# Performance work log

Measured on AMD Instinct MI355X. Metric: run time of the kernel, lower is better.

The kernel has to match this reference:

```python
import jax, jax.numpy as jnp
import numpy as np

N_WIN = 8
NUM_HEADS = 8
TOPK = 4
D_MODEL = 128
SCALE = D_MODEL ** (-0.5)


def setup_inputs() -> dict:
    key = jax.random.key(0)
    k1, k2 = jax.random.split(key)
    cv_feature = jax.random.normal(k1, (1, 128, 128, 128), dtype=jnp.float32)
    mv_feature = jax.random.normal(k2, (1, 2, 128, 128, 128), dtype=jnp.float32)
    return {"cv_feature": cv_feature, "mv_feature": mv_feature}


def reference(cv_feature, mv_feature):
    # cv_feature: [N, H, W, C] query view; mv_feature: [N, V, H, W, C] multi-view KV
    N, H, W, C = cv_feature.shape
    V = mv_feature.shape[1]
    j = i = N_WIN
    h, w = H // j, W // i
    p2, w2 = j * i, h * w
    ch = C // NUM_HEADS  # per-head dim

    # window partition: n (j h) (i w) c -> n (j i) h w c
    cv_patch = cv_feature.reshape(N, j, h, i, w, C).transpose(0, 1, 3, 2, 4, 5).reshape(N, p2, h, w, C)
    mv_patch = mv_feature.reshape(N, V, j, h, i, w, C).transpose(0, 1, 2, 4, 3, 5, 6).reshape(N, V, p2, h, w, C)

    q_pix = cv_patch.reshape(N, p2, w2, C)          # [N, p2, w2, C]
    kv_pix = mv_patch.reshape(N, V, p2, w2, C)      # [N, V, p2, w2, C]

    # window-level descriptors (means) -> routing logits
    q_win = cv_patch.mean(axis=(2, 3))              # [N, p2, C]
    k_win = mv_patch.mean(axis=(3, 4))              # [N, V, p2, C]

    # TopK routing (detached in original; forward math identical)
    k_flat = k_win.reshape(N, V * p2, C)
    attn_logit = jnp.einsum('npc,nqc->npq', q_win * SCALE, k_flat)  # [N, p2, V*p2]
    topk_logit, r_idx = jax.lax.top_k(attn_logit, TOPK)
    r_weight = jax.nn.softmax(topk_logit, axis=-1)  # computed by module, unused downstream

    # KV gather of selected windows: [N, p2, topk, w2, C]
    kv_flat = kv_pix.reshape(N, V * p2, w2, C)
    kv_sel = kv_flat[jnp.arange(N)[:, None, None], r_idx]

    # per-window multi-head attention over topk*w2 gathered tokens
    q = q_pix.reshape(N, p2, w2, NUM_HEADS, ch)
    kv = kv_sel.reshape(N, p2, TOPK * w2, NUM_HEADS, ch)
    attn = jnp.einsum('npwmc,npxmc->npmwx', q * SCALE, kv)  # [N, p2, m, w2, topk*w2]
    attn = jax.nn.softmax(attn, axis=-1)
    out = jnp.einsum('npmwx,npxmc->npwmc', attn, kv)        # [N, p2, w2, m, ch]

    # merge windows back: n (j i) (h w) c -> n (j h) (i w) c
    out = out.reshape(N, j, i, h, w, C).transpose(0, 1, 3, 2, 4, 5).reshape(N, H, W, C)
    return out
```

## Files before the change

### kernel.cpp

```cpp
#include <hip/hip_runtime.h>

#define HH_ 128
#define WW_ 128
#define CC_ 128
#define P2 64
#define W2 256
#define NH 8
#define CH 16
#define NV 2
#define TOPK 4
#define SCALE 0.08838834764831845f
#define SCALE_L2E 0.1275216f
#define CLAMP_L2 28.8539f

typedef unsigned short u16;
typedef unsigned int   u32;
typedef short s8v __attribute__((ext_vector_type(8)));
typedef float f4  __attribute__((ext_vector_type(4)));

#if __has_builtin(__builtin_amdgcn_exp2f)
#define EXP2(x) __builtin_amdgcn_exp2f(x)
#else
#define EXP2(x) exp2f(x)
#endif

union FRAG { uint4 q; u32 u[4]; s8v v; };

__device__ float g_means[(P2 + NV * P2) * CC_];
__device__ int2  g_part[64];
__device__ int   g_mode;
__device__ int   g_amb;

__device__ inline u16 f2b(float v) {
    union { float f; u32 u; } x; x.f = v;
    u32 r = x.u + 0x7FFFu + ((x.u >> 16) & 1u);
    return (u16)(r >> 16);
}
__device__ inline float b2f(u16 h) {
    union { u32 u; float f; } x; x.u = (u32)h << 16; return x.f;
}
__device__ inline float h2f(u16 h) {
    u32 s = (h >> 15) & 1u, e = (h >> 10) & 31u, m = h & 1023u;
    float v;
    if (e == 0)       v = m * 5.9604644775e-8f;
    else if (e == 31) v = 65504.f;
    else { union { u32 u; float f; } x; x.u = ((e + 112u) << 23) | (m << 13); v = x.f; }
    return s ? -v : v;
}
__device__ inline u16 f2h(float v) {
    union { float f; u32 u; } x; x.f = v;
    u32 s = (x.u >> 16) & 0x8000u;
    int  e = (int)((x.u >> 23) & 0xFF) - 112;
    u32  m = x.u & 0x7FFFFF;
    if (e >= 31) return (u16)(s | 0x7BFF);
    if (e <= 0) {
        if (e < -10) return (u16)s;
        m |= 0x800000u;
        int sh = 14 - e;
        u32 r = m >> sh, rem = m & ((1u << sh) - 1u), half = 1u << (sh - 1);
        if (rem > half || (rem == half && (r & 1))) r++;
        return (u16)(s | r);
    }
    u32 r = ((u32)e << 10) | (m >> 13), rem = m & 0x1FFFu;
    if (rem > 0x1000u || (rem == 0x1000u && (r & 1))) r++;
    return (u16)(s | r);
}

__device__ inline u32 pkhi(float a, float b) {
    union { float f; u32 u; } xa, xb; xa.f = a; xb.f = b;
    return (xa.u >> 16) | (xb.u & 0xFFFF0000u);
}
__device__ inline float hipart(float a) {
    union { float f; u32 u; } x; x.f = a; x.u &= 0xFFFF0000u; return x.f;
}

template<int MODE>
__device__ inline float decode1(const void* __restrict__ src, int off) {
    if (MODE == 0) return ((const float*)src)[off];
    u16 h = ((const u16*)src)[off];
    return (MODE == 1) ? b2f(h) : h2f(h);
}

template<int MODE>
__device__ inline float4 loadf4(const void* __restrict__ src, int off) {
    if (MODE == 0) return *(const float4*)((const float*)src + off);
    uint2 v = *(const uint2*)((const u16*)src + off);
    float4 r;
    if (MODE == 1) {
        r.x = b2f((u16)v.x); r.y = b2f((u16)(v.x >> 16));
        r.z = b2f((u16)v.y); r.w = b2f((u16)(v.y >> 16));
    } else {
        r.x = h2f((u16)v.x); r.y = h2f((u16)(v.x >> 16));
        r.z = h2f((u16)v.y); r.w = h2f((u16)(v.y >> 16));
    }
    return r;
}

template<int MODE>
__device__ inline void store4t(void* __restrict__ out, int off, const float* __restrict__ r) {
    if (MODE == 0) {
        *(float4*)((float*)out + off) = make_float4(r[0], r[1], r[2], r[3]);
    } else if (MODE == 1) {
        u32 w0 = (u32)f2b(r[0]) | ((u32)f2b(r[1]) << 16);
        u32 w1 = (u32)f2b(r[2]) | ((u32)f2b(r[3]) << 16);
        *(uint2*)((u16*)out + off) = make_uint2(w0, w1);
    } else {
        u32 w0 = (u32)f2h(r[0]) | ((u32)f2h(r[1]) << 16);
        u32 w1 = (u32)f2h(r[2]) | ((u32)f2h(r[3]) << 16);
        *(uint2*)((u16*)out + off) = make_uint2(w0, w1);
    }
}

__global__ void detect_sample(const void* __restrict__ cv, int n) {
    __shared__ int bc[2];
    int tid = threadIdx.x, k = blockIdx.x;
    if (tid < 2) bc[tid] = 0;
    __syncthreads();
    int lim32 = n / 2;
    int lim16 = n / 2;
    u32 r = ((u32)(tid + k * 257) * 2654435761u);
    int j32 = (int)(r % (u32)lim32);
    float a = fabsf(((const float*)cv)[j32]);
    bool c0 = (a >= 1e-4f && a <= 1e4f);
    int j16 = 2 * (int)((r >> 8) % (u32)lim16);
    float b = fabsf(b2f(((const u16*)cv)[j16]));
    bool c1 = (b >= 1e-4f && b <= 1e4f);
    unsigned long long b0 = __ballot(c0);
    unsigned long long b1 = __ballot(c1);
    if ((tid & 63) == 0) {
        atomicAdd(&bc[0], __popcll(b0));
        atomicAdd(&bc[1], __popcll(b1));
    }
    __syncthreads();
    if (tid == 0) g_part[k] = make_int2(bc[0], bc[1]);
}

__global__ void detect_final() {
    int tid = threadIdx.x;
    int2 v = g_part[tid];
    int c0 = v.x, c1 = v.y;
#pragma unroll
    for (int off = 32; off >= 1; off >>= 1) {
        c0 += __shfl_down(c0, off);
        c1 += __shfl_down(c1, off);
    }
    if (tid == 0) {
        const float T = 256.f * 64.f;
        float f0 = c0 / T, f1 = c1 / T;
        int mode, amb = 0;
        if (f1 >= 0.85f) mode = 1;
        else if (f0 >= 0.80f) mode = 0;
        else mode = 2;
        if ((f1 > 0.60f && f1 < 0.85f) || (mode != 1 && f0 > 0.65f && f0 < 0.80f)) amb = 1;
        g_mode = mode; g_amb = amb;
    }
}

template<int MODE>
__device__ inline void wm_accum(const void* __restrict__ src, int voff, int jj, int ii,
                                int pc, int c0, float* __restrict__ acc) {
#pragma unroll
    for (int k = 0; k < 8; ++k) {
        int px = 8 * pc + k;
        int hh = px >> 4, ww = px & 15;
        int a = voff + ((jj * 16 + hh) * WW_ + ii * 16 + ww) * CC_ + c0;
        if (MODE == 0) {
            const float4* p4 = (const float4*)((const float*)src + a);
            float4 x = p4[0], y = p4[1];
            acc[0] += x.x; acc[1] += x.y; acc[2] += x.z; acc[3] += x.w;
            acc[4] += y.x; acc[5] += y.y; acc[6] += y.z; acc[7] += y.w;
        } else {
            uint4 v = *(const uint4*)((const u16*)src + a);
            u32 wd[4] = { v.x, v.y, v.z, v.w };
#pragma unroll
            for (int j = 0; j < 4; ++j) {
                u16 lo = (u16)(wd[j] & 0xFFFFu), hi = (u16)(wd[j] >> 16);
                acc[2 * j]     += (MODE == 1) ? b2f(lo) : h2f(lo);
                acc[2 * j + 1] += (MODE == 1) ? b2f(hi) : h2f(hi);
            }
        }
    }
}

__global__ __launch_bounds__(512) void win_mean_kernel(const void* __restrict__ cv,
                                                       const void* __restrict__ mv) {
    __shared__ float part[32][128];
    int mode = g_mode;
    int row = blockIdx.x, tid = threadIdx.x;
    int o = tid & 15, pc = tid >> 4;
    const void* src; int voff = 0; int p;
    if (row < P2) { p = row; src = cv; }
    else { int r = row - P2; voff = (r >> 6) * HH_ * WW_ * CC_; p = r & 63; src = mv; }
    int jj = p >> 3, ii = p & 7;
    int c0 = 8 * o;
    float acc[8];
#pragma unroll
    for (int j = 0; j < 8; ++j) acc[j] = 0.f;
    if (mode == 0)      wm_accum<0>(src, voff, jj, ii, pc, c0, acc);
    else if (mode == 1) wm_accum<1>(src, voff, jj, ii, pc, c0, acc);
    else                wm_accum<2>(src, voff, jj, ii, pc, c0, acc);
#pragma unroll
    for (int j = 0; j < 8; ++j) part[pc][c0 + j] = acc[j];
    __syncthreads();
    if (tid < 128) {
        float s = 0.f;
#pragma unroll
        for (int k = 0; k < 32; ++k) s += part[k][tid];
        g_means[row * CC_ + tid] = s * (1.0f / 256.0f);
    }
}

template<int MODE>
__device__ void attn_body(const void* __restrict__ cv, const void* __restrict__ mv,
                          void* __restrict__ out, int p, int m, int tid,
                          u32 (* __restrict__ kfrag)[64][4],
                          u32 (* __restrict__ vfrag)[64][4],
                          const int* __restrict__ rwin) {
    int jj = p >> 3, ii = p & 7;
    int wv = tid >> 6, l = tid & 63;
    int lg = l >> 4, lr = l & 15;

    FRAG qf1[2], qf2[2];
#pragma unroll
    for (int qi = 0; qi < 2; ++qi) {
        int qrow = wv * 32 + qi * 16 + lr;
        int hh = qrow >> 4, ww = qrow & 15;
        int pix = (jj * 16 + hh) * WW_ + (ii * 16 + ww);
        float4 qv = loadf4<MODE>(cv, pix * CC_ + m * CH + 4 * lg);
        float q0 = qv.x * SCALE_L2E, q1 = qv.y * SCALE_L2E;
        float q2 = qv.z * SCALE_L2E, q3 = qv.w * SCALE_L2E;
        u32 h01 = pkhi(q0, q1), h23 = pkhi(q2, q3);
        u32 l01 = pkhi(q0 - hipart(q0), q1 - hipart(q1));
        u32 l23 = pkhi(q2 - hipart(q2), q3 - hipart(q3));
        qf1[qi].u[0] = h01; qf1[qi].u[1] = h23; qf1[qi].u[2] = l01; qf1[qi].u[3] = l23;
        qf2[qi].u[0] = l01; qf2[qi].u[1] = l23; qf2[qi].u[2] = h01; qf2[qi].u[3] = h23;
    }

    int ktl0 = tid >> 6;
    float4 kraw[2];
    float  vraw[2][4];

    auto loadh = [&](int r) {
        int t = rwin[r]; int v = t >> 6, pp = t & 63;
        int jj2 = pp >> 3, ii2 = pp & 7;
        int wrow = (v * HH_ + jj2 * 16) * WW_ + ii2 * 16;
        int kbr = (wrow + lr) * CC_ + m * CH + 4 * lg;
        int vbr = (wrow + 4 * lg) * CC_ + m * CH + lr;
#pragma unroll
        for (int i = 0; i < 2; ++i) {
            int ktl = ktl0 + 8 * i;
            kraw[i] = loadf4<MODE>(mv, kbr + ktl * (WW_ * CC_));
        }
#pragma unroll
        for (int i = 0; i < 2; ++i) {
            int ktl = ktl0 + 8 * i;
            int a = vbr + ktl * (WW_ * CC_);
#pragma unroll
            for (int io = 0; io < 4; ++io)
                vraw[i][io] = decode1<MODE>(mv, a + io * CC_);
        }
    };

    auto writeh = [&]() {
#pragma unroll
        for (int i = 0; i < 2; ++i) {
            int ktl = ktl0 + 8 * i;
            float4 kc = kraw[i];
            FRAG kf;
            kf.u[0] = pkhi(kc.x, kc.y);
            kf.u[1] = pkhi(kc.z, kc.w);
            kf.u[2] = pkhi(kc.x - hipart(kc.x), kc.y - hipart(kc.y));
            kf.u[3] = pkhi(kc.z - hipart(kc.z), kc.w - hipart(kc.w));
            *(uint4*)&kfrag[ktl][l][0] = kf.q;
            float v0 = vraw[i][0], v1 = vraw[i][1], v2 = vraw[i][2], v3 = vraw[i][3];
            FRAG vf;
            vf.u[0] = pkhi(v0, v1);
            vf.u[1] = pkhi(v2, v3);
            vf.u[2] = pkhi(v0 - hipart(v0), v1 - hipart(v1));
            vf.u[3] = pkhi(v2 - hipart(v2), v3 - hipart(v3));
            *(uint4*)&vfrag[ktl][l][0] = vf.q;
        }
    };

    f4 Oacc0 = {0.f, 0.f, 0.f, 0.f};
    f4 Oacc1 = {0.f, 0.f, 0.f, 0.f};
    float lp0 = 0.f, lp1 = 0.f;
    const uint4* kp = (const uint4*)&kfrag[0][0][0] + l;
    const uint4* vp = (const uint4*)&vfrag[0][0][0] + l;

    auto computeh = [&]() {
#pragma unroll 4
        for (int ktl = 0; ktl < 16; ++ktl) {
            FRAG kf, vf;
            kf.q = kp[ktl * 64];
            vf.q = vp[ktl * 64];
            {
                f4 sc = {0.f, 0.f, 0.f, 0.f};
                sc = __builtin_amdgcn_mfma_f32_16x16x32_bf16(kf.v, qf1[0].v, sc, 0, 0, 0);
                sc = __builtin_amdgcn_mfma_f32_16x16x32_bf16(kf.v, qf2[0].v, sc, 0, 0, 0);
                float pe0 = EXP2(fminf(sc[0], CLAMP_L2));
                float pe1 = EXP2(fminf(sc[1], CLAMP_L2));
                float pe2 = EXP2(fminf(sc[2], CLAMP_L2));
                float pe3 = EXP2(fminf(sc[3], CLAMP_L2));
                lp0 += (hipart(pe0) + hipart(pe1)) + (hipart(pe2) + hipart(pe3));
                FRAG pf;
                pf.u[0] = pkhi(pe0, pe1);
                pf.u[1] = pkhi(pe2, pe3);
                pf.u[2] = pf.u[0];
                pf.u[3] = pf.u[1];
                Oacc0 = __builtin_amdgcn_mfma_f32_16x16x32_bf16(vf.v, pf.v, Oacc0, 0, 0, 0);
            }
            {
                f4 sc = {0.f, 0.f, 0.f, 0.f};
                sc = __builtin_amdgcn_mfma_f32_16x16x32_bf16(kf.v, qf1[1].v, sc, 0, 0, 0);
                sc = __builtin_amdgcn_mfma_f32_16x16x32_bf16(kf.v, qf2[1].v, sc, 0, 0, 0);
                float pe0 = EXP2(fminf(sc[0], CLAMP_L2));
                float pe1 = EXP2(fminf(sc[1], CLAMP_L2));
                float pe2 = EXP2(fminf(sc[2], CLAMP_L2));
                float pe3 = EXP2(fminf(sc[3], CLAMP_L2));
                lp1 += (hipart(pe0) + hipart(pe1)) + (hipart(pe2) + hipart(pe3));
                FRAG pf;
                pf.u[0] = pkhi(pe0, pe1);
                pf.u[1] = pkhi(pe2, pe3);
                pf.u[2] = pf.u[0];
                pf.u[3] = pf.u[1];
                Oacc1 = __builtin_amdgcn_mfma_f32_16x16x32_bf16(vf.v, pf.v, Oacc1, 0, 0, 0);
            }
        }
    };

    loadh(0);
    writeh();
    __syncthreads();
#pragma unroll 1
    for (int r = 1; r < 4; ++r) {
        loadh(r);
        computeh();
        __syncthreads();
        writeh();
        __syncthreads();
    }
    computeh();

#pragma unroll
    for (int qi = 0; qi < 2; ++qi) {
        float lt = (qi == 0) ? lp0 : lp1;
        lt += __shfl_xor(lt, 16);
        lt += __shfl_xor(lt, 32);
        float inv = 1.0f / fmaxf(lt, 1e-30f);
        f4 Oa = (qi == 0) ? Oacc0 : Oacc1;
        float res[4];
#pragma unroll
        for (int r = 0; r < 4; ++r)
            res[r] = fminf(fmaxf(Oa[r] * inv, -1000.f), 1000.f);
        int qrow = wv * 32 + qi * 16 + lr;
        int hh = qrow >> 4, ww = qrow & 15;
        int pix = (jj * 16 + hh) * WW_ + (ii * 16 + ww);
        store4t<MODE>(out, pix * CC_ + m * CH + 4 * lg, res);
    }
}

__global__ __launch_bounds__(512, 6) void attn_kernel(const void* __restrict__ cv,
                                                      const void* __restrict__ mv,
                                                      void* __restrict__ out) {
    __shared__ u32 kfrag[16][64][4];
    __shared__ u32 vfrag[16][64][4];
    __shared__ float slog[NV * P2];
    __shared__ int   sridx[TOPK];

    int mode = g_mode;
    int p = blockIdx.x >> 3, m = blockIdx.x & 7;
    int tid = threadIdx.x;

    {
        int t  = tid >> 2;
        int cs = (tid & 3) << 5;
        const float4* qw = (const float4*)(g_means + p * CC_ + cs);
        const float4* kw = (const float4*)(g_means + (P2 + t) * CC_ + cs);
        float a = 0.f;
#pragma unroll
        for (int i = 0; i < 8; ++i) {
            float4 qv = qw[i], kv4 = kw[i];
            a += qv.x * kv4.x + qv.y * kv4.y + qv.z * kv4.z + qv.w * kv4.w;
        }
        a += __shfl_down(a, 2, 4);
        a += __shfl_down(a, 1, 4);
        if ((tid & 3) == 0) slog[t] = a;
    }
    __syncthreads();
    if (tid == 0) {
#pragma unroll
        for (int k = 0; k < TOPK; ++k) {
            int best = 0; float bv = slog[0];
            for (int q2 = 1; q2 < NV * P2; ++q2)
                if (slog[q2] > bv) { bv = slog[q2]; best = q2; }
            sridx[k] = best;
            slog[best] = -3.0e38f;
        }
    }
    __syncthreads();

    int rwin[TOPK];
#pragma unroll
    for (int k = 0; k < TOPK; ++k) rwin[k] = sridx[k] & 127;

    if (mode == 0)      attn_body<0>(cv, mv, out, p, m, tid, kfrag, vfrag, rwin);
    else if (mode == 1) attn_body<1>(cv, mv, out, p, m, tid, kfrag, vfrag, rwin);
    else                attn_body<2>(cv, mv, out, p, m, tid, kfrag, vfrag, rwin);
}

extern "C" void kernel_launch(void* const* d_in, const int* in_sizes, int n_in,
                              void* d_out, int out_size, void* d_ws, size_t ws_size,
                              hipStream_t stream) {
    const void* cv = d_in[0];
    const void* mv = d_in[1];
    int n_cv = in_sizes[0];
    if (n_in >= 2 && in_sizes[0] > in_sizes[1]) { cv = d_in[1]; mv = d_in[0]; n_cv = in_sizes[1]; }
    (void)d_ws; (void)ws_size; (void)out_size;

    detect_sample<<<64, 256, 0, stream>>>(cv, n_cv);
    detect_final<<<1, 64, 0, stream>>>();
    win_mean_kernel<<<192, 512, 0, stream>>>(cv, mv);
    attn_kernel<<<P2 * NH, 512, 0, stream>>>(cv, mv, d_out);
}
```

Before: 130.0 us.

## Split attention blocks over query quarters and fold mode detection into consumers

Attention blocks now each handle one quarter of a window's queries with 256 threads, giving four times as many blocks (2048 instead of 512). Each warp owns one 16-row query tile and streams keys in 8 half-window chunks, using two alternating output accumulators to break the MFMA dependency chain. The separate detect_final launch is removed, and every consumer block re-reduces the 64 detection partials itself. The cost is that each block reloads the same K/V data (four times the K/V global traffic) and recomputes routing logits and top-k redundantly.

```diff
diff --git a/kernel.cpp b/kernel.cpp
--- a/kernel.cpp
+++ b/kernel.cpp
@@ -28,8 +28,6 @@
 
 __device__ float g_means[(P2 + NV * P2) * CC_];
 __device__ int2  g_part[64];
-__device__ int   g_mode;
-__device__ int   g_amb;
 
 __device__ inline u16 f2b(float v) {
     union { float f; u32 u; } x; x.f = v;
@@ -72,6 +70,17 @@
 }
 __device__ inline float hipart(float a) {
     union { float f; u32 u; } x; x.f = a; x.u &= 0xFFFF0000u; return x.f;
+}
+
+__device__ inline int mode_from_parts() {
+    int c0 = 0, c1 = 0;
+#pragma unroll 8
+    for (int k = 0; k < 64; ++k) { int2 v = g_part[k]; c0 += v.x; c1 += v.y; }
+    const float T = 256.f * 64.f;
+    float f0 = c0 / T, f1 = c1 / T;
+    if (f1 >= 0.85f) return 1;
+    if (f0 >= 0.80f) return 0;
+    return 2;
 }
 
 template<int MODE>
@@ -135,27 +144,6 @@
     if (tid == 0) g_part[k] = make_int2(bc[0], bc[1]);
 }
 
-__global__ void detect_final() {
-    int tid = threadIdx.x;
-    int2 v = g_part[tid];
-    int c0 = v.x, c1 = v.y;
-#pragma unroll
-    for (int off = 32; off >= 1; off >>= 1) {
-        c0 += __shfl_down(c0, off);
-        c1 += __shfl_down(c1, off);
-    }
-    if (tid == 0) {
-        const float T = 256.f * 64.f;
-        float f0 = c0 / T, f1 = c1 / T;
-        int mode, amb = 0;
-        if (f1 >= 0.85f) mode = 1;
-        else if (f0 >= 0.80f) mode = 0;
-        else mode = 2;
-        if ((f1 > 0.60f && f1 < 0.85f) || (mode != 1 && f0 > 0.65f && f0 < 0.80f)) amb = 1;
-        g_mode = mode; g_amb = amb;
-    }
-}
-
 template<int MODE>
 __device__ inline void wm_accum(const void* __restrict__ src, int voff, int jj, int ii,
                                 int pc, int c0, float* __restrict__ acc) {
@@ -185,8 +173,11 @@
 __global__ __launch_bounds__(512) void win_mean_kernel(const void* __restrict__ cv,
                                                        const void* __restrict__ mv) {
     __shared__ float part[32][128];
-    int mode = g_mode;
+    __shared__ int   smode;
     int row = blockIdx.x, tid = threadIdx.x;
+    if (tid == 0) smode = mode_from_parts();
+    __syncthreads();
+    int mode = smode;
     int o = tid & 15, pc = tid >> 4;
     const void* src; int voff = 0; int p;
     if (row < P2) { p = row; src = cv; }
@@ -212,7 +203,7 @@
 
 template<int MODE>
 __device__ void attn_body(const void* __restrict__ cv, const void* __restrict__ mv,
-                          void* __restrict__ out, int p, int m, int tid,
+                          void* __restrict__ out, int p, int m, int qq, int tid,
                           u32 (* __restrict__ kfrag)[64][4],
                           u32 (* __restrict__ vfrag)[64][4],
                           const int* __restrict__ rwin) {
@@ -220,10 +211,9 @@
     int wv = tid >> 6, l = tid & 63;
     int lg = l >> 4, lr = l & 15;
 
-    FRAG qf1[2], qf2[2];
-#pragma unroll
-    for (int qi = 0; qi < 2; ++qi) {
-        int qrow = wv * 32 + qi * 16 + lr;
+    FRAG qf1, qf2;
+    {
+        int qrow = qq * 64 + wv * 16 + lr;
         int hh = qrow >> 4, ww = qrow & 15;
         int pix = (jj * 16 + hh) * WW_ + (ii * 16 + ww);
         float4 qv = loadf4<MODE>(cv, pix * CC_ + m * CH + 4 * lg);
@@ -232,29 +222,29 @@
         u32 h01 = pkhi(q0, q1), h23 = pkhi(q2, q3);
         u32 l01 = pkhi(q0 - hipart(q0), q1 - hipart(q1));
         u32 l23 = pkhi(q2 - hipart(q2), q3 - hipart(q3));
-        qf1[qi].u[0] = h01; qf1[qi].u[1] = h23; qf1[qi].u[2] = l01; qf1[qi].u[3] = l23;
-        qf2[qi].u[0] = l01; qf2[qi].u[1] = l23; qf2[qi].u[2] = h01; qf2[qi].u[3] = h23;
-    }
-
-    int ktl0 = tid >> 6;
+        qf1.u[0] = h01; qf1.u[1] = h23; qf1.u[2] = l01; qf1.u[3] = l23;
+        qf2.u[0] = l01; qf2.u[1] = l23; qf2.u[2] = h01; qf2.u[3] = h23;
+    }
+
+    int tl0 = tid >> 6;
     float4 kraw[2];
     float  vraw[2][4];
 
     auto loadh = [&](int r) {
-        int t = rwin[r]; int v = t >> 6, pp = t & 63;
+        int t = rwin[r >> 1]; int v = t >> 6, pp = t & 63;
         int jj2 = pp >> 3, ii2 = pp & 7;
-        int wrow = (v * HH_ + jj2 * 16) * WW_ + ii2 * 16;
+        int wrow = (v * HH_ + jj2 * 16 + (r & 1) * 8) * WW_ + ii2 * 16;
         int kbr = (wrow + lr) * CC_ + m * CH + 4 * lg;
         int vbr = (wrow + 4 * lg) * CC_ + m * CH + lr;
 #pragma unroll
         for (int i = 0; i < 2; ++i) {
-            int ktl = ktl0 + 8 * i;
-            kraw[i] = loadf4<MODE>(mv, kbr + ktl * (WW_ * CC_));
+            int tl = tl0 + 4 * i;
+            kraw[i] = loadf4<MODE>(mv, kbr + tl * (WW_ * CC_));
         }
 #pragma unroll
         for (int i = 0; i < 2; ++i) {
-            int ktl = ktl0 + 8 * i;
-            int a = vbr + ktl * (WW_ * CC_);
+            int tl = tl0 + 4 * i;
+            int a = vbr + tl * (WW_ * CC_);
 #pragma unroll
             for (int io = 0; io < 4; ++io)
                 vraw[i][io] = decode1<MODE>(mv, a + io * CC_);
@@ -264,68 +254,53 @@
     auto writeh = [&]() {
 #pragma unroll
         for (int i = 0; i < 2; ++i) {
-            int ktl = ktl0 + 8 * i;
+            int tl = tl0 + 4 * i;
             float4 kc = kraw[i];
             FRAG kf;
             kf.u[0] = pkhi(kc.x, kc.y);
             kf.u[1] = pkhi(kc.z, kc.w);
             kf.u[2] = pkhi(kc.x - hipart(kc.x), kc.y - hipart(kc.y));
             kf.u[3] = pkhi(kc.z - hipart(kc.z), kc.w - hipart(kc.w));
-            *(uint4*)&kfrag[ktl][l][0] = kf.q;
+            *(uint4*)&kfrag[tl][l][0] = kf.q;
             float v0 = vraw[i][0], v1 = vraw[i][1], v2 = vraw[i][2], v3 = vraw[i][3];
             FRAG vf;
             vf.u[0] = pkhi(v0, v1);
             vf.u[1] = pkhi(v2, v3);
             vf.u[2] = pkhi(v0 - hipart(v0), v1 - hipart(v1));
             vf.u[3] = pkhi(v2 - hipart(v2), v3 - hipart(v3));
-            *(uint4*)&vfrag[ktl][l][0] = vf.q;
+            *(uint4*)&vfrag[tl][l][0] = vf.q;
         }
     };
 
-    f4 Oacc0 = {0.f, 0.f, 0.f, 0.f};
-    f4 Oacc1 = {0.f, 0.f, 0.f, 0.f};
-    float lp0 = 0.f, lp1 = 0.f;
+    f4 OaccA = {0.f, 0.f, 0.f, 0.f};
+    f4 OaccB = {0.f, 0.f, 0.f, 0.f};
+    float lp = 0.f;
     const uint4* kp = (const uint4*)&kfrag[0][0][0] + l;
     const uint4* vp = (const uint4*)&vfrag[0][0][0] + l;
 
     auto computeh = [&]() {
 #pragma unroll 4
-        for (int ktl = 0; ktl < 16; ++ktl) {
+        for (int tl = 0; tl < 8; ++tl) {
             FRAG kf, vf;
-            kf.q = kp[ktl * 64];
-            vf.q = vp[ktl * 64];
-            {
-                f4 sc = {0.f, 0.f, 0.f, 0.f};
-                sc = __builtin_amdgcn_mfma_f32_16x16x32_bf16(kf.v, qf1[0].v, sc, 0, 0, 0);
-                sc = __builtin_amdgcn_mfma_f32_16x16x32_bf16(kf.v, qf2[0].v, sc, 0, 0, 0);
-                float pe0 = EXP2(fminf(sc[0], CLAMP_L2));
-                float pe1 = EXP2(fminf(sc[1], CLAMP_L2));
-                float pe2 = EXP2(fminf(sc[2], CLAMP_L2));
-                float pe3 = EXP2(fminf(sc[3], CLAMP_L2));
-                lp0 += (hipart(pe0) + hipart(pe1)) + (hipart(pe2) + hipart(pe3));
-                FRAG pf;
-                pf.u[0] = pkhi(pe0, pe1);
-                pf.u[1] = pkhi(pe2, pe3);
-                pf.u[2] = pf.u[0];
-                pf.u[3] = pf.u[1];
-                Oacc0 = __builtin_amdgcn_mfma_f32_16x16x32_bf16(vf.v, pf.v, Oacc0, 0, 0, 0);
-            }
-            {
-                f4 sc = {0.f, 0.f, 0.f, 0.f};
-                sc = __builtin_amdgcn_mfma_f32_16x16x32_bf16(kf.v, qf1[1].v, sc, 0, 0, 0);
-                sc = __builtin_amdgcn_mfma_f32_16x16x32_bf16(kf.v, qf2[1].v, sc, 0, 0, 0);
-                float pe0 = EXP2(fminf(sc[0], CLAMP_L2));
-                float pe1 = EXP2(fminf(sc[1], CLAMP_L2));
-                float pe2 = EXP2(fminf(sc[2], CLAMP_L2));
-                float pe3 = EXP2(fminf(sc[3], CLAMP_L2));
-                lp1 += (hipart(pe0) + hipart(pe1)) + (hipart(pe2) + hipart(pe3));
-                FRAG pf;
-                pf.u[0] = pkhi(pe0, pe1);
-                pf.u[1] = pkhi(pe2, pe3);
-                pf.u[2] = pf.u[0];
-                pf.u[3] = pf.u[1];
-                Oacc1 = __builtin_amdgcn_mfma_f32_16x16x32_bf16(vf.v, pf.v, Oacc1, 0, 0, 0);
-            }
+            kf.q = kp[tl * 64];
+            vf.q = vp[tl * 64];
+            f4 sc = {0.f, 0.f, 0.f, 0.f};
+            sc = __builtin_amdgcn_mfma_f32_16x16x32_bf16(kf.v, qf1.v, sc, 0, 0, 0);
+            sc = __builtin_amdgcn_mfma_f32_16x16x32_bf16(kf.v, qf2.v, sc, 0, 0, 0);
+            float pe0 = EXP2(fminf(sc[0], CLAMP_L2));
+            float pe1 = EXP2(fminf(sc[1], CLAMP_L2));
+            float pe2 = EXP2(fminf(sc[2], CLAMP_L2));
+            float pe3 = EXP2(fminf(sc[3], CLAMP_L2));
+            lp += (hipart(pe0) + hipart(pe1)) + (hipart(pe2) + hipart(pe3));
+            FRAG pf;
+            pf.u[0] = pkhi(pe0, pe1);
+            pf.u[1] = pkhi(pe2, pe3);
+            pf.u[2] = pf.u[0];
+            pf.u[3] = pf.u[1];
+            if (tl & 1)
+                OaccB = __builtin_amdgcn_mfma_f32_16x16x32_bf16(vf.v, pf.v, OaccB, 0, 0, 0);
+            else
+                OaccA = __builtin_amdgcn_mfma_f32_16x16x32_bf16(vf.v, pf.v, OaccA, 0, 0, 0);
         }
     };
 
@@ -333,7 +308,7 @@
     writeh();
     __syncthreads();
 #pragma unroll 1
-    for (int r = 1; r < 4; ++r) {
+    for (int r = 1; r < 8; ++r) {
         loadh(r);
         computeh();
         __syncthreads();
@@ -342,53 +317,50 @@
     }
     computeh();
 
-#pragma unroll
-    for (int qi = 0; qi < 2; ++qi) {
-        float lt = (qi == 0) ? lp0 : lp1;
-        lt += __shfl_xor(lt, 16);
-        lt += __shfl_xor(lt, 32);
-        float inv = 1.0f / fmaxf(lt, 1e-30f);
-        f4 Oa = (qi == 0) ? Oacc0 : Oacc1;
-        float res[4];
-#pragma unroll
-        for (int r = 0; r < 4; ++r)
-            res[r] = fminf(fmaxf(Oa[r] * inv, -1000.f), 1000.f);
-        int qrow = wv * 32 + qi * 16 + lr;
-        int hh = qrow >> 4, ww = qrow & 15;
-        int pix = (jj * 16 + hh) * WW_ + (ii * 16 + ww);
-        store4t<MODE>(out, pix * CC_ + m * CH + 4 * lg, res);
-    }
-}
-
-__global__ __launch_bounds__(512, 6) void attn_kernel(const void* __restrict__ cv,
+    float lt = lp;
+    lt += __shfl_xor(lt, 16);
+    lt += __shfl_xor(lt, 32);
+    float inv = 1.0f / fmaxf(lt, 1e-30f);
+    float res[4];
+#pragma unroll
+    for (int r = 0; r < 4; ++r)
+        res[r] = fminf(fmaxf((OaccA[r] + OaccB[r]) * inv, -1000.f), 1000.f);
+    int qrow = qq * 64 + wv * 16 + lr;
+    int hh = qrow >> 4, ww = qrow & 15;
+    int pix = (jj * 16 + hh) * WW_ + (ii * 16 + ww);
+    store4t<MODE>(out, pix * CC_ + m * CH + 4 * lg, res);
+}
+
+__global__ __launch_bounds__(256, 6) void attn_kernel(const void* __restrict__ cv,
                                                       const void* __restrict__ mv,
                                                       void* __restrict__ out) {
-    __shared__ u32 kfrag[16][64][4];
-    __shared__ u32 vfrag[16][64][4];
+    __shared__ u32 kfrag[8][64][4];
+    __shared__ u32 vfrag[8][64][4];
     __shared__ float slog[NV * P2];
     __shared__ int   sridx[TOPK];
-
-    int mode = g_mode;
-    int p = blockIdx.x >> 3, m = blockIdx.x & 7;
+    __shared__ int   smode;
+
+    int bid = blockIdx.x;
+    int qq = bid & 3, m = (bid >> 2) & 7, p = bid >> 5;
     int tid = threadIdx.x;
 
     {
-        int t  = tid >> 2;
-        int cs = (tid & 3) << 5;
+        int t  = tid >> 1;
+        int cs = (tid & 1) << 6;
         const float4* qw = (const float4*)(g_means + p * CC_ + cs);
         const float4* kw = (const float4*)(g_means + (P2 + t) * CC_ + cs);
         float a = 0.f;
 #pragma unroll
-        for (int i = 0; i < 8; ++i) {
+        for (int i = 0; i < 16; ++i) {
             float4 qv = qw[i], kv4 = kw[i];
             a += qv.x * kv4.x + qv.y * kv4.y + qv.z * kv4.z + qv.w * kv4.w;
         }
-        a += __shfl_down(a, 2, 4);
-        a += __shfl_down(a, 1, 4);
-        if ((tid & 3) == 0) slog[t] = a;
+        a += __shfl_down(a, 1, 2);
+        if ((tid & 1) == 0) slog[t] = a;
     }
     __syncthreads();
     if (tid == 0) {
+        smode = mode_from_parts();
 #pragma unroll
         for (int k = 0; k < TOPK; ++k) {
             int best = 0; float bv = slog[0];
@@ -400,13 +372,14 @@
     }
     __syncthreads();
 
+    int mode = smode;
     int rwin[TOPK];
 #pragma unroll
     for (int k = 0; k < TOPK; ++k) rwin[k] = sridx[k] & 127;
 
-    if (mode == 0)      attn_body<0>(cv, mv, out, p, m, tid, kfrag, vfrag, rwin);
-    else if (mode == 1) attn_body<1>(cv, mv, out, p, m, tid, kfrag, vfrag, rwin);
-    else                attn_body<2>(cv, mv, out, p, m, tid, kfrag, vfrag, rwin);
+    if (mode == 0)      attn_body<0>(cv, mv, out, p, m, qq, tid, kfrag, vfrag, rwin);
+    else if (mode == 1) attn_body<1>(cv, mv, out, p, m, qq, tid, kfrag, vfrag, rwin);
+    else                attn_body<2>(cv, mv, out, p, m, qq, tid, kfrag, vfrag, rwin);
 }
 
 extern "C" void kernel_launch(void* const* d_in, const int* in_sizes, int n_in,
@@ -419,7 +392,6 @@
     (void)d_ws; (void)ws_size; (void)out_size;
 
     detect_sample<<<64, 256, 0, stream>>>(cv, n_cv);
-    detect_final<<<1, 64, 0, stream>>>();
     win_mean_kernel<<<192, 512, 0, stream>>>(cv, mv);
-    attn_kernel<<<P2 * NH, 512, 0, stream>>>(cv, mv, d_out);
-}
+    attn_kernel<<<P2 * NH * 4, 256, 0, stream>>>(cv, mv, d_out);
+}
```

Result: slower. 151.9 us (+16.8%).

## Split KV across two wave groups with 1024-thread blocks and drop detect_final

Applied to the files above, without the earlier changes.

The attention kernel now runs 1024 threads per block. Two halves of the waves each process half of the gathered key tiles per stage, so the four staged KV rounds become two. The partial outputs and softmax sums are merged through shared memory before the store. The separate detect_final launch is removed, and each block recomputes the dtype mode from the 64 partial counts. This cuts one kernel launch and the serial stage syncs, at the cost of doubled shared memory, an extra combine step and lower occupancy per block.

```diff
diff --git a/kernel.cpp b/kernel.cpp
--- a/kernel.cpp
+++ b/kernel.cpp
@@ -28,8 +28,6 @@
 
 __device__ float g_means[(P2 + NV * P2) * CC_];
 __device__ int2  g_part[64];
-__device__ int   g_mode;
-__device__ int   g_amb;
 
 __device__ inline u16 f2b(float v) {
     union { float f; u32 u; } x; x.f = v;
@@ -72,6 +70,17 @@
 }
 __device__ inline float hipart(float a) {
     union { float f; u32 u; } x; x.f = a; x.u &= 0xFFFF0000u; return x.f;
+}
+
+__device__ inline int mode_from_parts() {
+    int c0 = 0, c1 = 0;
+#pragma unroll 8
+    for (int k = 0; k < 64; ++k) { int2 v = g_part[k]; c0 += v.x; c1 += v.y; }
+    const float T = 256.f * 64.f;
+    float f0 = c0 / T, f1 = c1 / T;
+    if (f1 >= 0.85f) return 1;
+    if (f0 >= 0.80f) return 0;
+    return 2;
 }
 
 template<int MODE>
@@ -135,27 +144,6 @@
     if (tid == 0) g_part[k] = make_int2(bc[0], bc[1]);
 }
 
-__global__ void detect_final() {
-    int tid = threadIdx.x;
-    int2 v = g_part[tid];
-    int c0 = v.x, c1 = v.y;
-#pragma unroll
-    for (int off = 32; off >= 1; off >>= 1) {
-        c0 += __shfl_down(c0, off);
-        c1 += __shfl_down(c1, off);
-    }
-    if (tid == 0) {
-        const float T = 256.f * 64.f;
-        float f0 = c0 / T, f1 = c1 / T;
-        int mode, amb = 0;
-        if (f1 >= 0.85f) mode = 1;
-        else if (f0 >= 0.80f) mode = 0;
-        else mode = 2;
-        if ((f1 > 0.60f && f1 < 0.85f) || (mode != 1 && f0 > 0.65f && f0 < 0.80f)) amb = 1;
-        g_mode = mode; g_amb = amb;
-    }
-}
-
 template<int MODE>
 __device__ inline void wm_accum(const void* __restrict__ src, int voff, int jj, int ii,
                                 int pc, int c0, float* __restrict__ acc) {
@@ -185,8 +173,11 @@
 __global__ __launch_bounds__(512) void win_mean_kernel(const void* __restrict__ cv,
                                                        const void* __restrict__ mv) {
     __shared__ float part[32][128];
-    int mode = g_mode;
+    __shared__ int   smode;
     int row = blockIdx.x, tid = threadIdx.x;
+    if (tid == 0) smode = mode_from_parts();
+    __syncthreads();
+    int mode = smode;
     int o = tid & 15, pc = tid >> 4;
     const void* src; int voff = 0; int p;
     if (row < P2) { p = row; src = cv; }
@@ -218,12 +209,13 @@
                           const int* __restrict__ rwin) {
     int jj = p >> 3, ii = p & 7;
     int wv = tid >> 6, l = tid & 63;
+    int kh = wv >> 3, qs = wv & 7;
     int lg = l >> 4, lr = l & 15;
 
     FRAG qf1[2], qf2[2];
 #pragma unroll
     for (int qi = 0; qi < 2; ++qi) {
-        int qrow = wv * 32 + qi * 16 + lr;
+        int qrow = qs * 32 + qi * 16 + lr;
         int hh = qrow >> 4, ww = qrow & 15;
         int pix = (jj * 16 + hh) * WW_ + (ii * 16 + ww);
         float4 qv = loadf4<MODE>(cv, pix * CC_ + m * CH + 4 * lg);
@@ -236,25 +228,21 @@
         qf2[qi].u[0] = l01; qf2[qi].u[1] = l23; qf2[qi].u[2] = h01; qf2[qi].u[3] = h23;
     }
 
-    int ktl0 = tid >> 6;
     float4 kraw[2];
     float  vraw[2][4];
 
     auto loadh = [&](int r) {
-        int t = rwin[r]; int v = t >> 6, pp = t & 63;
-        int jj2 = pp >> 3, ii2 = pp & 7;
-        int wrow = (v * HH_ + jj2 * 16) * WW_ + ii2 * 16;
-        int kbr = (wrow + lr) * CC_ + m * CH + 4 * lg;
-        int vbr = (wrow + 4 * lg) * CC_ + m * CH + lr;
 #pragma unroll
         for (int i = 0; i < 2; ++i) {
-            int ktl = ktl0 + 8 * i;
-            kraw[i] = loadf4<MODE>(mv, kbr + ktl * (WW_ * CC_));
-        }
-#pragma unroll
-        for (int i = 0; i < 2; ++i) {
-            int ktl = ktl0 + 8 * i;
-            int a = vbr + ktl * (WW_ * CC_);
+            int s = tid + i * 1024;
+            int tl = s >> 6, sl = s & 63;
+            int slg = sl >> 4, slr = sl & 15;
+            int t = rwin[2 * r + (tl >> 4)];
+            int v = t >> 6, pp = t & 63;
+            int jj2 = pp >> 3, ii2 = pp & 7;
+            int wrow = (v * HH_ + jj2 * 16 + (tl & 15)) * WW_ + ii2 * 16;
+            kraw[i] = loadf4<MODE>(mv, (wrow + slr) * CC_ + m * CH + 4 * slg);
+            int a = (wrow + 4 * slg) * CC_ + m * CH + slr;
 #pragma unroll
             for (int io = 0; io < 4; ++io)
                 vraw[i][io] = decode1<MODE>(mv, a + io * CC_);
@@ -264,36 +252,37 @@
     auto writeh = [&]() {
 #pragma unroll
         for (int i = 0; i < 2; ++i) {
-            int ktl = ktl0 + 8 * i;
+            int s = tid + i * 1024;
+            int tl = s >> 6, sl = s & 63;
             float4 kc = kraw[i];
             FRAG kf;
             kf.u[0] = pkhi(kc.x, kc.y);
             kf.u[1] = pkhi(kc.z, kc.w);
             kf.u[2] = pkhi(kc.x - hipart(kc.x), kc.y - hipart(kc.y));
             kf.u[3] = pkhi(kc.z - hipart(kc.z), kc.w - hipart(kc.w));
-            *(uint4*)&kfrag[ktl][l][0] = kf.q;
+            *(uint4*)&kfrag[tl][sl][0] = kf.q;
             float v0 = vraw[i][0], v1 = vraw[i][1], v2 = vraw[i][2], v3 = vraw[i][3];
             FRAG vf;
             vf.u[0] = pkhi(v0, v1);
             vf.u[1] = pkhi(v2, v3);
             vf.u[2] = pkhi(v0 - hipart(v0), v1 - hipart(v1));
             vf.u[3] = pkhi(v2 - hipart(v2), v3 - hipart(v3));
-            *(uint4*)&vfrag[ktl][l][0] = vf.q;
+            *(uint4*)&vfrag[tl][sl][0] = vf.q;
         }
     };
 
     f4 Oacc0 = {0.f, 0.f, 0.f, 0.f};
     f4 Oacc1 = {0.f, 0.f, 0.f, 0.f};
     float lp0 = 0.f, lp1 = 0.f;
-    const uint4* kp = (const uint4*)&kfrag[0][0][0] + l;
-    const uint4* vp = (const uint4*)&vfrag[0][0][0] + l;
+    const uint4* kp = (const uint4*)&kfrag[kh * 16][0][0] + l;
+    const uint4* vp = (const uint4*)&vfrag[kh * 16][0][0] + l;
 
     auto computeh = [&]() {
 #pragma unroll 4
-        for (int ktl = 0; ktl < 16; ++ktl) {
+        for (int tl = 0; tl < 16; ++tl) {
             FRAG kf, vf;
-            kf.q = kp[ktl * 64];
-            vf.q = vp[ktl * 64];
+            kf.q = kp[tl * 64];
+            vf.q = vp[tl * 64];
             {
                 f4 sc = {0.f, 0.f, 0.f, 0.f};
                 sc = __builtin_amdgcn_mfma_f32_16x16x32_bf16(kf.v, qf1[0].v, sc, 0, 0, 0);
@@ -332,63 +321,79 @@
     loadh(0);
     writeh();
     __syncthreads();
-#pragma unroll 1
-    for (int r = 1; r < 4; ++r) {
-        loadh(r);
-        computeh();
-        __syncthreads();
-        writeh();
-        __syncthreads();
-    }
+    loadh(1);
     computeh();
-
-#pragma unroll
-    for (int qi = 0; qi < 2; ++qi) {
-        float lt = (qi == 0) ? lp0 : lp1;
-        lt += __shfl_xor(lt, 16);
-        lt += __shfl_xor(lt, 32);
-        float inv = 1.0f / fmaxf(lt, 1e-30f);
-        f4 Oa = (qi == 0) ? Oacc0 : Oacc1;
-        float res[4];
-#pragma unroll
-        for (int r = 0; r < 4; ++r)
-            res[r] = fminf(fmaxf(Oa[r] * inv, -1000.f), 1000.f);
-        int qrow = wv * 32 + qi * 16 + lr;
-        int hh = qrow >> 4, ww = qrow & 15;
-        int pix = (jj * 16 + hh) * WW_ + (ii * 16 + ww);
-        store4t<MODE>(out, pix * CC_ + m * CH + 4 * lg, res);
-    }
-}
-
-__global__ __launch_bounds__(512, 6) void attn_kernel(const void* __restrict__ cv,
-                                                      const void* __restrict__ mv,
-                                                      void* __restrict__ out) {
-    __shared__ u32 kfrag[16][64][4];
-    __shared__ u32 vfrag[16][64][4];
+    __syncthreads();
+    writeh();
+    __syncthreads();
+    computeh();
+    __syncthreads();
+
+    float* comb = (float*)&kfrag[0][0][0];
+    int ci = (qs * 64 + l) * 10;
+    if (kh == 1) {
+#pragma unroll
+        for (int r = 0; r < 4; ++r) { comb[ci + r] = Oacc0[r]; comb[ci + 4 + r] = Oacc1[r]; }
+        comb[ci + 8] = lp0;
+        comb[ci + 9] = lp1;
+    }
+    __syncthreads();
+    if (kh == 0) {
+#pragma unroll
+        for (int r = 0; r < 4; ++r) { Oacc0[r] += comb[ci + r]; Oacc1[r] += comb[ci + 4 + r]; }
+        lp0 += comb[ci + 8];
+        lp1 += comb[ci + 9];
+#pragma unroll
+        for (int qi = 0; qi < 2; ++qi) {
+            float lt = (qi == 0) ? lp0 : lp1;
+            lt += __shfl_xor(lt, 16);
+            lt += __shfl_xor(lt, 32);
+            float inv = 1.0f / fmaxf(lt, 1e-30f);
+            f4 Oa = (qi == 0) ? Oacc0 : Oacc1;
+            float res[4];
+#pragma unroll
+            for (int r = 0; r < 4; ++r)
+                res[r] = fminf(fmaxf(Oa[r] * inv, -1000.f), 1000.f);
+            int qrow = qs * 32 + qi * 16 + lr;
+            int hh = qrow >> 4, ww = qrow & 15;
+            int pix = (jj * 16 + hh) * WW_ + (ii * 16 + ww);
+            store4t<MODE>(out, pix * CC_ + m * CH + 4 * lg, res);
+        }
+    }
+}
+
+__global__ __launch_bounds__(1024, 8) void attn_kernel(const void* __restrict__ cv,
+                                                       const void* __restrict__ mv,
+                                                       void* __restrict__ out) {
+    __shared__ u32 kfrag[32][64][4];
+    __shared__ u32 vfrag[32][64][4];
     __shared__ float slog[NV * P2];
     __shared__ int   sridx[TOPK];
-
-    int mode = g_mode;
-    int p = blockIdx.x >> 3, m = blockIdx.x & 7;
+    __shared__ int   smode;
+
+    int bid = blockIdx.x;
+    int p = bid >> 3, m = bid & 7;
     int tid = threadIdx.x;
 
     {
-        int t  = tid >> 2;
-        int cs = (tid & 3) << 5;
+        int t  = tid >> 3;
+        int cs = (tid & 7) << 4;
         const float4* qw = (const float4*)(g_means + p * CC_ + cs);
         const float4* kw = (const float4*)(g_means + (P2 + t) * CC_ + cs);
         float a = 0.f;
 #pragma unroll
-        for (int i = 0; i < 8; ++i) {
+        for (int i = 0; i < 4; ++i) {
             float4 qv = qw[i], kv4 = kw[i];
             a += qv.x * kv4.x + qv.y * kv4.y + qv.z * kv4.z + qv.w * kv4.w;
         }
-        a += __shfl_down(a, 2, 4);
-        a += __shfl_down(a, 1, 4);
-        if ((tid & 3) == 0) slog[t] = a;
+        a += __shfl_down(a, 4, 8);
+        a += __shfl_down(a, 2, 8);
+        a += __shfl_down(a, 1, 8);
+        if ((tid & 7) == 0) slog[t] = a;
     }
     __syncthreads();
     if (tid == 0) {
+        smode = mode_from_parts();
 #pragma unroll
         for (int k = 0; k < TOPK; ++k) {
             int best = 0; float bv = slog[0];
@@ -400,6 +405,7 @@
     }
     __syncthreads();
 
+    int mode = smode;
     int rwin[TOPK];
 #pragma unroll
     for (int k = 0; k < TOPK; ++k) rwin[k] = sridx[k] & 127;
@@ -419,7 +425,6 @@
     (void)d_ws; (void)ws_size; (void)out_size;
 
     detect_sample<<<64, 256, 0, stream>>>(cv, n_cv);
-    detect_final<<<1, 64, 0, stream>>>();
     win_mean_kernel<<<192, 512, 0, stream>>>(cv, mv);
-    attn_kernel<<<P2 * NH, 512, 0, stream>>>(cv, mv, d_out);
-}
+    attn_kernel<<<P2 * NH, 1024, 0, stream>>>(cv, mv, d_out);
+}
```

Result: slower. 135.5 us (+4.2%).
